# Optimization experiments

Measured on AMD Instinct MI355X. Metric: run time of the kernel, lower is better.

## Reference

```python
import jax, jax.numpy as jnp
import numpy as np

T = 0.2
EPS = 1e-05


def setup_inputs() -> dict:
    key = jax.random.key(0)
    k1, k2 = jax.random.split(key)
    N, D, NUM_CLASSES = 8192, 128, 128
    inp = jax.random.normal(k1, (N, D), dtype=jnp.float32)
    label = jax.random.randint(k2, (N,), 0, NUM_CLASSES, dtype=jnp.int64)
    return {"input": inp, "label": label}


def reference(input, label):
    # Pairwise cosine similarity: dot(x_i, x_j) / max(||x_i|| * ||x_j||, eps)
    norms = jnp.sqrt(jnp.sum(input * input, axis=1))            # [N]
    denom = jnp.maximum(norms[:, None] * norms[None, :], EPS)   # [N, N]
    sim = (input @ input.T) / denom                             # [N, N]

    mask = (label[:, None] == label[None, :]).astype(input.dtype)  # same-label mask
    e = jnp.exp(sim / T)
    e = e - jnp.diag(jnp.diag(e))                               # zero the diagonal

    pos = mask * e                                              # positives (diag already 0)
    unsim = jnp.sum(e - pos, axis=-1, keepdims=True)            # [N, 1] negatives row-sum
    ratio = pos / (pos + unsim)                                 # per-pair NT-Xent prob
    safe = jnp.where(ratio > 0, ratio, 1.0)                     # loss[loss<=0] = 1
    loss_sum = jnp.sum(-jnp.log(safe))

    # number of off-diagonal positive pairs
    off_diag_mask = mask - jnp.diag(jnp.diag(mask))
    n_pos = jnp.count_nonzero(off_diag_mask).astype(input.dtype)
    return loss_sum / n_pos
```

## Files before the change

### kernel.cpp

```cpp
#include <hip/hip_runtime.h>
#include <math.h>

typedef float f32x4 __attribute__((ext_vector_type(4)));
typedef __attribute__((address_space(3))) unsigned int lds_u32;
typedef __attribute__((address_space(1))) const unsigned int glb_u32;

__global__ __launch_bounds__(256) void norm_kernel(
    const float* __restrict__ X, unsigned char* __restrict__ Y8,
    float* __restrict__ unsim, float* __restrict__ psum,
    float* __restrict__ accum, float inv_sqrtT) {
  int t = threadIdx.x;
  int row = blockIdx.x * 8 + (t >> 5);
  int l32 = t & 31;
  float4 v = ((const float4*)(X + (size_t)row * 128))[l32];
  float s = v.x * v.x + v.y * v.y + v.z * v.z + v.w * v.w;
  s += __shfl_xor(s, 1);
  s += __shfl_xor(s, 2);
  s += __shfl_xor(s, 4);
  s += __shfl_xor(s, 8);
  s += __shfl_xor(s, 16);
  float inv = inv_sqrtT * rsqrtf(fmaxf(s, 1e-24f));
  int pk = __builtin_amdgcn_cvt_pk_fp8_f32(v.x * inv, v.y * inv, 0, false);
  pk = __builtin_amdgcn_cvt_pk_fp8_f32(v.z * inv, v.w * inv, pk, true);
  int chunk = l32 >> 2;
  int off = ((chunk ^ (row & 7)) << 4) + ((l32 & 3) << 2);
  *(unsigned int*)(Y8 + (size_t)row * 128 + off) = (unsigned)pk;
  if (t < 8) unsim[blockIdx.x * 8 + t] = 0.f;
  else if (t < 16) psum[blockIdx.x * 8 + (t - 8)] = 0.f;
  if (blockIdx.x == 0 && t >= 224 && t < 232) accum[t - 224] = 0.f;
}

__global__ __launch_bounds__(256, 4) void pass1_kernel(
    const unsigned char* __restrict__ Y8, const int* __restrict__ lab,
    float* __restrict__ unsim, float* __restrict__ psumG,
    float* __restrict__ accum, int nt) {
  __shared__ unsigned char As[128][128];
  __shared__ unsigned char Bs[128][128];
  __shared__ int labR[128], labC[128];
  __shared__ float tsumS[128], tcolS[128];
  __shared__ float psumS[256];
  __shared__ float diagS[128];
  __shared__ float sS[4];

  int b = blockIdx.x;
  float ntf = (float)nt;
  int bi = (int)((2.f * ntf + 1.f -
                  sqrtf((2.f * ntf + 1.f) * (2.f * ntf + 1.f) - 8.f * (float)b)) *
                 0.5f);
  if (bi < 0) bi = 0;
  while ((bi + 1) * nt - ((bi + 1) * bi) / 2 <= b) ++bi;
  while (bi * nt - (bi * (bi - 1)) / 2 > b) --bi;
  int bj = bi + (b - (bi * nt - (bi * (bi - 1)) / 2));
  const int i0 = bi * 128, j0 = bj * 128;
  const bool offdiag = (bi != bj);

  const int t = threadIdx.x;
  const int w = t >> 6, lane = t & 63;

#pragma unroll
  for (int k = 0; k < 4; ++k) {
    const int c0 = w * 64 + k * 256;
    const int c = c0 + lane;
    __builtin_amdgcn_global_load_lds(
        (glb_u32*)(Y8 + (size_t)i0 * 128 + (size_t)c * 16),
        (lds_u32*)((unsigned char*)&As[0][0] + c0 * 16), 16, 0, 0);
    __builtin_amdgcn_global_load_lds(
        (glb_u32*)(Y8 + (size_t)j0 * 128 + (size_t)c * 16),
        (lds_u32*)((unsigned char*)&Bs[0][0] + c0 * 16), 16, 0, 0);
  }
  if (t < 128) {
    labR[t] = lab[i0 + t];
    tsumS[t] = 0.f;
    psumS[t] = 0.f;
    diagS[t] = 0.f;
  } else {
    labC[t - 128] = lab[j0 + t - 128];
    tcolS[t - 128] = 0.f;
    psumS[t] = 0.f;
  }
  __syncthreads();

  const int quad = lane >> 4, l16 = lane & 15;
  const int rbase = w * 32;
  const int sw = l16 & 7;

  f32x4 acc[2][8] = {};
#pragma unroll
  for (int ks = 0; ks < 4; ++ks) {
    const int ch = ks * 2 + (quad >> 1);
    const int off = ((ch ^ sw) << 4) + ((quad & 1) << 3);
    long af[2], bf[8];
#pragma unroll
    for (int p = 0; p < 2; ++p)
      af[p] = *(const long*)&As[rbase + p * 16 + l16][off];
#pragma unroll
    for (int p = 0; p < 8; ++p)
      bf[p] = *(const long*)&Bs[p * 16 + l16][off];
#pragma unroll
    for (int pi = 0; pi < 2; ++pi)
#pragma unroll
      for (int pj = 0; pj < 8; ++pj)
        acc[pi][pj] = __builtin_amdgcn_mfma_f32_16x16x32_fp8_fp8(
            af[pi], bf[pj], acc[pi][pj], 0, 0, 0);
  }

  int lr[2][4], lc[8];
#pragma unroll
  for (int pi = 0; pi < 2; ++pi)
#pragma unroll
    for (int r = 0; r < 4; ++r) lr[pi][r] = labR[rbase + pi * 16 + quad * 4 + r];
#pragma unroll
  for (int pj = 0; pj < 8; ++pj) lc[pj] = labC[pj * 16 + l16];

  float trow[2][4] = {};
  float tcol[8] = {};
  float sacc = 0.f;
#pragma unroll
  for (int pi = 0; pi < 2; ++pi)
#pragma unroll
    for (int pj = 0; pj < 8; ++pj)
#pragma unroll
      for (int r = 0; r < 4; ++r) {
        const float s = acc[pi][pj][r];
        const float e = __expf(s);
        trow[pi][r] += e;
        tcol[pj] += e;
        if (lr[pi][r] == lc[pj]) {
          const int row = rbase + pi * 16 + quad * 4 + r;
          const int col = pj * 16 + l16;
          if (offdiag) {
            atomicAdd(&psumS[row], e);
            atomicAdd(&psumS[128 + col], e);
            sacc += 2.f * s;
          } else if (row != col) {
            atomicAdd(&psumS[row], e);
            sacc += s;
          } else {
            diagS[row] = e;
          }
        }
      }

#pragma unroll
  for (int pi = 0; pi < 2; ++pi)
#pragma unroll
    for (int r = 0; r < 4; ++r) {
      float v = trow[pi][r];
      v += __shfl_xor(v, 1);
      v += __shfl_xor(v, 2);
      v += __shfl_xor(v, 4);
      v += __shfl_xor(v, 8);
      if (l16 == 0) tsumS[rbase + pi * 16 + quad * 4 + r] = v;
    }
#pragma unroll
  for (int pj = 0; pj < 8; ++pj) {
    float v = tcol[pj];
    v += __shfl_xor(v, 16);
    v += __shfl_xor(v, 32);
    if (quad == 0) atomicAdd(&tcolS[pj * 16 + l16], v);
  }
#pragma unroll
  for (int m = 1; m < 64; m <<= 1) sacc += __shfl_xor(sacc, m);
  if (lane == 0) sS[w] = sacc;
  __syncthreads();

  if (t < 128) {
    atomicAdd(&unsim[i0 + t], tsumS[t] - diagS[t]);
    atomicAdd(&psumG[i0 + t], psumS[t]);
  } else if (offdiag) {
    atomicAdd(&unsim[j0 + (t - 128)], tcolS[t - 128]);
    atomicAdd(&psumG[j0 + (t - 128)], psumS[t]);
  }
  if (t == 0) {
    atomicAdd(&accum[4], sS[0] + sS[1] + sS[2] + sS[3]);
  }
}

__global__ __launch_bounds__(1024) void finalize_kernel(
    const int* __restrict__ lab, const float* __restrict__ unsim,
    const float* __restrict__ psum, const float* __restrict__ accum,
    float* __restrict__ out, int N) {
  __shared__ int hist[256];
  __shared__ float redL[16], redN[16];
  int t = threadIdx.x;
  int lane = t & 63, w = t >> 6;
  if (t < 256) hist[t] = 0;
  __syncthreads();
  for (int i = t; i < N; i += 1024) atomicAdd(&hist[lab[i] & 255], 1);
  __syncthreads();
  float local = 0.f;
  for (int i = t; i < N; i += 1024) {
    float tot = unsim[i];
    float p = psum[i];
    float u = tot - p;
    float c = (float)(hist[lab[i] & 255] - 1);
    local += c * __logf(u) + p / u;
  }
  float nposl = 0.f;
  if (t < 256) {
    float m = (float)hist[t];
    nposl = m * m;
  }
#pragma unroll
  for (int msk = 1; msk < 64; msk <<= 1) {
    local += __shfl_xor(local, msk);
    nposl += __shfl_xor(nposl, msk);
  }
  if (lane == 0) {
    redL[w] = local;
    redN[w] = nposl;
  }
  __syncthreads();
  if (t == 0) {
    float ls = 0.f, np = 0.f;
#pragma unroll
    for (int i = 0; i < 16; ++i) {
      ls += redL[i];
      np += redN[i];
    }
    out[0] = (ls - accum[4]) / (np - (float)N);
  }
}

extern "C" void kernel_launch(void* const* d_in, const int* in_sizes, int n_in,
                              void* d_out, int out_size, void* d_ws,
                              size_t ws_size, hipStream_t stream) {
  const float* X = (const float*)d_in[0];
  const int* lab = (const int*)d_in[1];
  float* out = (float*)d_out;

  const int N = in_sizes[1];

  unsigned char* Y8 = (unsigned char*)d_ws;
  float* unsim = (float*)(Y8 + (size_t)N * 128);
  float* psum = unsim + N;
  float* accum = psum + N;

  const float inv_sqrtT = 2.2360679775f;
  norm_kernel<<<N / 8, 256, 0, stream>>>(X, Y8, unsim, psum, accum,
                                         inv_sqrtT);

  const int nt = N / 128;
  const int nblk = nt * (nt + 1) / 2;
  pass1_kernel<<<nblk, 256, 0, stream>>>(Y8, lab, unsim, psum, accum, nt);
  finalize_kernel<<<1, 1024, 0, stream>>>(lab, unsim, psum, accum, out, N);
}
```

Baseline: 104.9 us.

## Replace symmetric triangular tiling with full row-strip tiles and double-buffered B loads

The pass kernel stops exploiting symmetry of the similarity matrix. Each block now owns a 128-row strip and loops over 8 column tiles, double-buffering the B tile in LDS while keeping A fragments in registers. Global atomics are replaced by per-chunk partial arrays that the finalize kernel reduces, which also removes the zero-initialisation in the norm kernel. This doubles the MFMA and exp work compared with the triangular scheme, in exchange for dropping column reductions, global atomics, triangular index math and per-block load latency. Occupancy hint drops from 4 to 2 blocks per CU.

```diff
diff --git a/kernel.cpp b/kernel.cpp
--- a/kernel.cpp
+++ b/kernel.cpp
@@ -7,8 +7,7 @@
 
 __global__ __launch_bounds__(256) void norm_kernel(
     const float* __restrict__ X, unsigned char* __restrict__ Y8,
-    float* __restrict__ unsim, float* __restrict__ psum,
-    float* __restrict__ accum, float inv_sqrtT) {
+    float inv_sqrtT) {
   int t = threadIdx.x;
   int row = blockIdx.x * 8 + (t >> 5);
   int l32 = t & 31;
@@ -25,58 +24,39 @@
   int chunk = l32 >> 2;
   int off = ((chunk ^ (row & 7)) << 4) + ((l32 & 3) << 2);
   *(unsigned int*)(Y8 + (size_t)row * 128 + off) = (unsigned)pk;
-  if (t < 8) unsim[blockIdx.x * 8 + t] = 0.f;
-  else if (t < 16) psum[blockIdx.x * 8 + (t - 8)] = 0.f;
-  if (blockIdx.x == 0 && t >= 224 && t < 232) accum[t - 224] = 0.f;
-}
-
-__global__ __launch_bounds__(256, 4) void pass1_kernel(
+}
+
+__global__ __launch_bounds__(256, 2) void pass1_kernel(
     const unsigned char* __restrict__ Y8, const int* __restrict__ lab,
-    float* __restrict__ unsim, float* __restrict__ psumG,
-    float* __restrict__ accum, int nt) {
+    float* __restrict__ P, float* __restrict__ Q, float* __restrict__ S,
+    int N) {
   __shared__ unsigned char As[128][128];
-  __shared__ unsigned char Bs[128][128];
-  __shared__ int labR[128], labC[128];
-  __shared__ float tsumS[128], tcolS[128];
-  __shared__ float psumS[256];
-  __shared__ float diagS[128];
+  __shared__ unsigned char Bs[2][128][128];
+  __shared__ int labR[128];
+  __shared__ float tsumS[128], psumS[128], diagS[128];
   __shared__ float sS[4];
 
-  int b = blockIdx.x;
-  float ntf = (float)nt;
-  int bi = (int)((2.f * ntf + 1.f -
-                  sqrtf((2.f * ntf + 1.f) * (2.f * ntf + 1.f) - 8.f * (float)b)) *
-                 0.5f);
-  if (bi < 0) bi = 0;
-  while ((bi + 1) * nt - ((bi + 1) * bi) / 2 <= b) ++bi;
-  while (bi * nt - (bi * (bi - 1)) / 2 > b) --bi;
-  int bj = bi + (b - (bi * nt - (bi * (bi - 1)) / 2));
-  const int i0 = bi * 128, j0 = bj * 128;
-  const bool offdiag = (bi != bj);
-
+  const int b = blockIdx.x;
+  const int bi = b >> 3, c = b & 7;
+  const int i0 = bi * 128;
   const int t = threadIdx.x;
   const int w = t >> 6, lane = t & 63;
 
 #pragma unroll
   for (int k = 0; k < 4; ++k) {
     const int c0 = w * 64 + k * 256;
-    const int c = c0 + lane;
+    const int cc = c0 + lane;
     __builtin_amdgcn_global_load_lds(
-        (glb_u32*)(Y8 + (size_t)i0 * 128 + (size_t)c * 16),
+        (glb_u32*)(Y8 + (size_t)i0 * 128 + (size_t)cc * 16),
         (lds_u32*)((unsigned char*)&As[0][0] + c0 * 16), 16, 0, 0);
     __builtin_amdgcn_global_load_lds(
-        (glb_u32*)(Y8 + (size_t)j0 * 128 + (size_t)c * 16),
-        (lds_u32*)((unsigned char*)&Bs[0][0] + c0 * 16), 16, 0, 0);
+        (glb_u32*)(Y8 + (size_t)(c * 8) * 128 * 128 + (size_t)cc * 16),
+        (lds_u32*)((unsigned char*)&Bs[0][0][0] + c0 * 16), 16, 0, 0);
   }
   if (t < 128) {
     labR[t] = lab[i0 + t];
-    tsumS[t] = 0.f;
     psumS[t] = 0.f;
     diagS[t] = 0.f;
-  } else {
-    labC[t - 128] = lab[j0 + t - 128];
-    tcolS[t - 128] = 0.f;
-    psumS[t] = 0.f;
   }
   __syncthreads();
 
@@ -84,62 +64,87 @@
   const int rbase = w * 32;
   const int sw = l16 & 7;
 
-  f32x4 acc[2][8] = {};
+  long af[4][2];
 #pragma unroll
   for (int ks = 0; ks < 4; ++ks) {
     const int ch = ks * 2 + (quad >> 1);
     const int off = ((ch ^ sw) << 4) + ((quad & 1) << 3);
-    long af[2], bf[8];
 #pragma unroll
     for (int p = 0; p < 2; ++p)
-      af[p] = *(const long*)&As[rbase + p * 16 + l16][off];
-#pragma unroll
-    for (int p = 0; p < 8; ++p)
-      bf[p] = *(const long*)&Bs[p * 16 + l16][off];
+      af[ks][p] = *(const long*)&As[rbase + p * 16 + l16][off];
+  }
+  int lr[2][4];
+#pragma unroll
+  for (int pi = 0; pi < 2; ++pi)
+#pragma unroll
+    for (int r = 0; r < 4; ++r)
+      lr[pi][r] = labR[rbase + pi * 16 + quad * 4 + r];
+
+  float trow[2][4] = {};
+  float sacc = 0.f;
+
+#pragma unroll 2
+  for (int jt = 0; jt < 8; ++jt) {
+    const int cur = jt & 1;
+    const int jtile = c * 8 + jt;
+    const int jt0 = jtile * 128;
+
+    if (jt < 7) {
+      const unsigned char* src = Y8 + (size_t)(jt0 + 128) * 128;
+      unsigned char* dst = (unsigned char*)&Bs[cur ^ 1][0][0];
+#pragma unroll
+      for (int k = 0; k < 4; ++k) {
+        const int c0 = w * 64 + k * 256;
+        const int cc = c0 + lane;
+        __builtin_amdgcn_global_load_lds((glb_u32*)(src + (size_t)cc * 16),
+                                         (lds_u32*)(dst + c0 * 16), 16, 0, 0);
+      }
+    }
+
+    int lc[8];
+#pragma unroll
+    for (int pj = 0; pj < 8; ++pj) lc[pj] = lab[jt0 + pj * 16 + l16];
+
+    f32x4 acc[2][8] = {};
+#pragma unroll
+    for (int ks = 0; ks < 4; ++ks) {
+      const int ch = ks * 2 + (quad >> 1);
+      const int off = ((ch ^ sw) << 4) + ((quad & 1) << 3);
+      long bf[8];
+#pragma unroll
+      for (int p = 0; p < 8; ++p)
+        bf[p] = *(const long*)&Bs[cur][p * 16 + l16][off];
+#pragma unroll
+      for (int pi = 0; pi < 2; ++pi)
+#pragma unroll
+        for (int pj = 0; pj < 8; ++pj)
+          acc[pi][pj] = __builtin_amdgcn_mfma_f32_16x16x32_fp8_fp8(
+              af[ks][pi], bf[pj], acc[pi][pj], 0, 0, 0);
+    }
+
+    const bool dtile = (jtile == bi);
 #pragma unroll
     for (int pi = 0; pi < 2; ++pi)
 #pragma unroll
       for (int pj = 0; pj < 8; ++pj)
-        acc[pi][pj] = __builtin_amdgcn_mfma_f32_16x16x32_fp8_fp8(
-            af[pi], bf[pj], acc[pi][pj], 0, 0, 0);
-  }
-
-  int lr[2][4], lc[8];
-#pragma unroll
-  for (int pi = 0; pi < 2; ++pi)
-#pragma unroll
-    for (int r = 0; r < 4; ++r) lr[pi][r] = labR[rbase + pi * 16 + quad * 4 + r];
-#pragma unroll
-  for (int pj = 0; pj < 8; ++pj) lc[pj] = labC[pj * 16 + l16];
-
-  float trow[2][4] = {};
-  float tcol[8] = {};
-  float sacc = 0.f;
-#pragma unroll
-  for (int pi = 0; pi < 2; ++pi)
-#pragma unroll
-    for (int pj = 0; pj < 8; ++pj)
-#pragma unroll
-      for (int r = 0; r < 4; ++r) {
-        const float s = acc[pi][pj][r];
-        const float e = __expf(s);
-        trow[pi][r] += e;
-        tcol[pj] += e;
-        if (lr[pi][r] == lc[pj]) {
-          const int row = rbase + pi * 16 + quad * 4 + r;
-          const int col = pj * 16 + l16;
-          if (offdiag) {
-            atomicAdd(&psumS[row], e);
-            atomicAdd(&psumS[128 + col], e);
-            sacc += 2.f * s;
-          } else if (row != col) {
-            atomicAdd(&psumS[row], e);
-            sacc += s;
-          } else {
-            diagS[row] = e;
+#pragma unroll
+        for (int r = 0; r < 4; ++r) {
+          const float s = acc[pi][pj][r];
+          const float e = __expf(s);
+          trow[pi][r] += e;
+          if (lr[pi][r] == lc[pj]) {
+            const int rowl = rbase + pi * 16 + quad * 4 + r;
+            const int cl = pj * 16 + l16;
+            if (dtile && rowl == cl) {
+              diagS[rowl] = e;
+            } else {
+              atomicAdd(&psumS[rowl], e);
+              sacc += s;
+            }
           }
         }
-      }
+    __syncthreads();
+  }
 
 #pragma unroll
   for (int pi = 0; pi < 2; ++pi)
@@ -153,35 +158,24 @@
       if (l16 == 0) tsumS[rbase + pi * 16 + quad * 4 + r] = v;
     }
 #pragma unroll
-  for (int pj = 0; pj < 8; ++pj) {
-    float v = tcol[pj];
-    v += __shfl_xor(v, 16);
-    v += __shfl_xor(v, 32);
-    if (quad == 0) atomicAdd(&tcolS[pj * 16 + l16], v);
-  }
-#pragma unroll
   for (int m = 1; m < 64; m <<= 1) sacc += __shfl_xor(sacc, m);
   if (lane == 0) sS[w] = sacc;
   __syncthreads();
 
   if (t < 128) {
-    atomicAdd(&unsim[i0 + t], tsumS[t] - diagS[t]);
-    atomicAdd(&psumG[i0 + t], psumS[t]);
-  } else if (offdiag) {
-    atomicAdd(&unsim[j0 + (t - 128)], tcolS[t - 128]);
-    atomicAdd(&psumG[j0 + (t - 128)], psumS[t]);
-  }
-  if (t == 0) {
-    atomicAdd(&accum[4], sS[0] + sS[1] + sS[2] + sS[3]);
-  }
+    const int gi = i0 + t;
+    P[c * N + gi] = tsumS[t] - diagS[t];
+    Q[c * N + gi] = psumS[t];
+  }
+  if (t == 0) S[b] = sS[0] + sS[1] + sS[2] + sS[3];
 }
 
 __global__ __launch_bounds__(1024) void finalize_kernel(
-    const int* __restrict__ lab, const float* __restrict__ unsim,
-    const float* __restrict__ psum, const float* __restrict__ accum,
+    const int* __restrict__ lab, const float* __restrict__ P,
+    const float* __restrict__ Q, const float* __restrict__ S,
     float* __restrict__ out, int N) {
   __shared__ int hist[256];
-  __shared__ float redL[16], redN[16];
+  __shared__ float redL[16], redN[16], redS[16];
   int t = threadIdx.x;
   int lane = t & 63, w = t >> 6;
   if (t < 256) hist[t] = 0;
@@ -190,35 +184,43 @@
   __syncthreads();
   float local = 0.f;
   for (int i = t; i < N; i += 1024) {
-    float tot = unsim[i];
-    float p = psum[i];
+    float tot = 0.f, p = 0.f;
+#pragma unroll
+    for (int cc = 0; cc < 8; ++cc) {
+      tot += P[cc * N + i];
+      p += Q[cc * N + i];
+    }
     float u = tot - p;
-    float c = (float)(hist[lab[i] & 255] - 1);
-    local += c * __logf(u) + p / u;
+    float cnt = (float)(hist[lab[i] & 255] - 1);
+    local += cnt * __logf(u) + p / u;
   }
   float nposl = 0.f;
   if (t < 256) {
     float m = (float)hist[t];
     nposl = m * m;
   }
+  float sl = (t < 512) ? S[t] : 0.f;
 #pragma unroll
   for (int msk = 1; msk < 64; msk <<= 1) {
     local += __shfl_xor(local, msk);
     nposl += __shfl_xor(nposl, msk);
+    sl += __shfl_xor(sl, msk);
   }
   if (lane == 0) {
     redL[w] = local;
     redN[w] = nposl;
+    redS[w] = sl;
   }
   __syncthreads();
   if (t == 0) {
-    float ls = 0.f, np = 0.f;
+    float ls = 0.f, np = 0.f, ss = 0.f;
 #pragma unroll
     for (int i = 0; i < 16; ++i) {
       ls += redL[i];
       np += redN[i];
-    }
-    out[0] = (ls - accum[4]) / (np - (float)N);
+      ss += redS[i];
+    }
+    out[0] = (ls - ss) / (np - (float)N);
   }
 }
 
@@ -232,16 +234,14 @@
   const int N = in_sizes[1];
 
   unsigned char* Y8 = (unsigned char*)d_ws;
-  float* unsim = (float*)(Y8 + (size_t)N * 128);
-  float* psum = unsim + N;
-  float* accum = psum + N;
+  float* P = (float*)(Y8 + (size_t)N * 128);
+  float* Q = P + 8 * (size_t)N;
+  float* S = Q + 8 * (size_t)N;
 
   const float inv_sqrtT = 2.2360679775f;
-  norm_kernel<<<N / 8, 256, 0, stream>>>(X, Y8, unsim, psum, accum,
-                                         inv_sqrtT);
-
-  const int nt = N / 128;
-  const int nblk = nt * (nt + 1) / 2;
-  pass1_kernel<<<nblk, 256, 0, stream>>>(Y8, lab, unsim, psum, accum, nt);
-  finalize_kernel<<<1, 1024, 0, stream>>>(lab, unsim, psum, accum, out, N);
-}
+  norm_kernel<<<N / 8, 256, 0, stream>>>(X, Y8, inv_sqrtT);
+
+  const int nblk = (N / 128) * 8;
+  pass1_kernel<<<nblk, 256, 0, stream>>>(Y8, lab, P, Q, S, N);
+  finalize_kernel<<<1, 1024, 0, stream>>>(lab, P, Q, S, out, N);
+}
```

After: 98.47 us. 6.1% less time.
